# Kernel optimization log

Measured on AMD Instinct MI355X. Metric: run time of the kernel, lower is better.

## Reference

```python
import jax, jax.numpy as jnp
import numpy as np

N_NODES = 100000
N_EDGES = 1600000
N_GRAPHS = 1024
DIM_IN = 128
DIM_SELF = 16
BN_EPS = 1e-5


def _bn(x, gamma, beta):
    # training-mode BatchNorm1d over dim 0 (biased variance, as torch uses for normalization)
    m = jnp.mean(x, axis=0)
    v = jnp.mean((x - m) ** 2, axis=0)
    return gamma * (x - m) * jax.lax.rsqrt(v + BN_EPS) + beta


def _mlp(x, W1, b1, g, b, W2, b2):
    h = x @ W1 + b1
    h = jax.nn.relu(_bn(h, g, b))
    return h @ W2 + b2


def _gin(h, src, dst, W1, b1, g, b, W2, b2):
    # GINConv with eps=0: (1+eps)*h + sum over in-neighbors, then MLP
    agg = jax.ops.segment_sum(h[src], dst, num_segments=N_NODES)
    return _mlp(h + agg, W1, b1, g, b, W2, b2)


def setup_inputs() -> dict:
    key = jax.random.key(0)
    ks = jax.random.split(key, 16)

    def lin(k, fan_in, fan_out):
        bound = 1.0 / np.sqrt(fan_in)
        k1, k2 = jax.random.split(k)
        W = jax.random.uniform(k1, (fan_in, fan_out), jnp.float32, -bound, bound)
        b = jax.random.uniform(k2, (fan_out,), jnp.float32, -bound, bound)
        return W, b

    inp = {}
    inp['feat'] = jax.random.normal(ks[0], (N_NODES, DIM_IN), jnp.float32)
    inp['self_feat'] = jax.random.normal(ks[1], (N_GRAPHS, DIM_SELF), jnp.float32)
    inp['edge_src'] = jax.random.randint(ks[2], (N_EDGES,), 0, N_NODES, jnp.int32)
    inp['edge_dst'] = jax.random.randint(ks[3], (N_EDGES,), 0, N_NODES, jnp.int32)
    inp['node2graph'] = jnp.sort(jax.random.randint(ks[4], (N_NODES,), 0, N_GRAPHS, jnp.int32))

    inp['g1_W1'], inp['g1_b1'] = lin(ks[5], DIM_IN, 100)
    inp['g1_gamma'] = jnp.ones((100,), jnp.float32)
    inp['g1_beta'] = jnp.zeros((100,), jnp.float32)
    inp['g1_W2'], inp['g1_b2'] = lin(ks[6], 100, 100)

    inp['g2_W1'], inp['g2_b1'] = lin(ks[7], 100, 20)
    inp['g2_gamma'] = jnp.ones((20,), jnp.float32)
    inp['g2_beta'] = jnp.zeros((20,), jnp.float32)
    inp['g2_W2'], inp['g2_b2'] = lin(ks[8], 20, 20)

    inp['fc1_W'], inp['fc1_b'] = lin(ks[9], 20 * DIM_SELF, 32)
    inp['bn1_gamma'] = jnp.ones((32,), jnp.float32)
    inp['bn1_beta'] = jnp.zeros((32,), jnp.float32)
    inp['fc2_W'], inp['fc2_b'] = lin(ks[10], 32, 8)
    inp['bn2_gamma'] = jnp.ones((8,), jnp.float32)
    inp['bn2_beta'] = jnp.zeros((8,), jnp.float32)
    inp['fc3_W'], inp['fc3_b'] = lin(ks[11], 8, 1)
    return inp


def reference(feat, self_feat,
              g1_W1, g1_b1, g1_gamma, g1_beta, g1_W2, g1_b2,
              g2_W1, g2_b1, g2_gamma, g2_beta, g2_W2, g2_b2,
              fc1_W, fc1_b, bn1_gamma, bn1_beta,
              fc2_W, fc2_b, bn2_gamma, bn2_beta,
              fc3_W, fc3_b,
              edge_src, edge_dst, node2graph):
    h = _gin(feat, edge_src, edge_dst, g1_W1, g1_b1, g1_gamma, g1_beta, g1_W2, g1_b2)
    h = jax.nn.relu(h)
    h = _gin(h, edge_src, edge_dst, g2_W1, g2_b1, g2_gamma, g2_beta, g2_W2, g2_b2)
    h = jax.nn.relu(h)  # [N, 20]

    # dgl.mean_nodes: per-graph mean of node features
    sums = jax.ops.segment_sum(h, node2graph, num_segments=N_GRAPHS)  # [B, 20]
    cnts = jax.ops.segment_sum(jnp.ones((N_NODES,), h.dtype), node2graph, num_segments=N_GRAPHS)
    hg = sums / jnp.maximum(cnts, 1.0)[:, None]

    # kronecker fusion: bmm([B,20,1],[B,1,dim_self]) -> flatten
    kron = jnp.einsum('bi,bj->bij', hg, self_feat).reshape(N_GRAPHS, -1)  # [B, 20*dim_self]

    out = jax.nn.relu(_bn(kron @ fc1_W + fc1_b, bn1_gamma, bn1_beta))
    # dropout(0.3) is identity in eval mode
    out = jax.nn.relu(_bn(out @ fc2_W + fc2_b, bn2_gamma, bn2_beta))
    out = out @ fc3_W + fc3_b  # [B, dim_out]
    return out
```

## Files before the change

### kernel.cpp

```cpp
#include <hip/hip_runtime.h>

#define NN 100000
#define NE 1600000
#define NG 1024
#define DIN 128
#define D1 100
#define D2 20
#define DSELF 16
#define BN_EPS 1e-5f

#define NB 391
#define NBLK 782
#define EPB 2048
#define RAWCAP 5120
#define NAGG2 4000
#define NREP 64
#define APITCH 136

typedef unsigned int uint;
typedef unsigned short ushort;
typedef __attribute__((ext_vector_type(8))) short bfv8;
typedef __attribute__((ext_vector_type(4))) float fv4;

__device__ inline float bflo(uint x) { return __uint_as_float(x << 16); }
__device__ inline float bfhi(uint x) { return __uint_as_float(x & 0xffff0000u); }
__device__ inline float bfval(ushort h) { return __uint_as_float(((uint)h) << 16); }
__device__ inline uint packbf2(float a, float b) {
    uint ua = __float_as_uint(a), ub = __float_as_uint(b);
    ua += 0x7fffu + ((ua >> 16) & 1u);
    ub += 0x7fffu + ((ub >> 16) & 1u);
    return (ua >> 16) | (ub & 0xffff0000u);
}
__device__ inline ushort bfr(float x) {
    uint u = __float_as_uint(x);
    u += 0x7fffu + ((u >> 16) & 1u);
    return (ushort)(u >> 16);
}

__global__ __launch_bounds__(256) void k_gemm1(const float* __restrict__ feat,
                                               const float* __restrict__ W1,
                                               ushort* __restrict__ z1bf,
                                               float* __restrict__ pb1r) {
    __shared__ __align__(16) char smem[64 * APITCH * 2 + 112 * APITCH * 2];
    ushort* Al = (ushort*)smem;
    ushort* Bt = (ushort*)(smem + 64 * APITCH * 2);
    int t = threadIdx.x;
    if (blockIdx.x == 0) {
        for (int i = t; i < NREP * 200; i += 256) pb1r[i] = 0.f;
    }
    int row0 = blockIdx.x * 64;
#pragma unroll
    for (int i = 0; i < 8; i++) {
        int p = i * 256 + t;
        int r = p >> 5, cq = p & 31;
        int row = row0 + r; if (row >= NN) row = NN - 1;
        float4 v = *(const float4*)(feat + (size_t)row * DIN + cq * 4);
        ushort* dst = Al + r * APITCH + 4 * cq;
        dst[0] = bfr(v.x); dst[1] = bfr(v.y); dst[2] = bfr(v.z); dst[3] = bfr(v.w);
    }
    for (int p = t; p < 12800; p += 256) {
        int k = p / 100, n = p % 100;
        Bt[n * APITCH + k] = bfr(W1[p]);
    }
    __syncthreads();
    int w = __builtin_amdgcn_readfirstlane(t >> 6);
    int l = t & 63;
    int m16 = l & 15, quad = l >> 4;
    fv4 acc[7];
#pragma unroll
    for (int nt = 0; nt < 7; nt++) acc[nt] = (fv4){0.f, 0.f, 0.f, 0.f};
    const ushort* arow = Al + (w * 16 + m16) * APITCH;
#pragma unroll
    for (int kk = 0; kk < 4; kk++) {
        int kb = kk * 32 + quad * 8;
        bfv8 a = *(const bfv8*)(arow + kb);
#pragma unroll
        for (int nt = 0; nt < 7; nt++) {
            bfv8 b = *(const bfv8*)(Bt + (nt * 16 + m16) * APITCH + kb);
            acc[nt] = __builtin_amdgcn_mfma_f32_16x16x32_bf16(a, b, acc[nt], 0, 0, 0);
        }
    }
    __syncthreads();
    float* Ep = (float*)smem;
#pragma unroll
    for (int nt = 0; nt < 7; nt++) {
        int n = nt * 16 + m16;
        if (n < 100) {
#pragma unroll
            for (int rix = 0; rix < 4; rix++)
                Ep[(w * 16 + quad * 4 + rix) * 101 + n] = acc[nt][rix];
        }
    }
    __syncthreads();
#pragma unroll
    for (int i = 0; i < 13; i++) {
        int p = i * 256 + t;
        if (p < 3200) {
            int rr = p / 50, cc = 2 * (p % 50);
            int row = row0 + rr;
            if (row < NN) {
                float v0 = Ep[rr * 101 + cc], v1 = Ep[rr * 101 + cc + 1];
                *(uint*)(z1bf + (size_t)row * 128 + cc) = packbf2(v0, v1);
            }
        }
    }
}

__global__ __launch_bounds__(256) void k_csrA1(const int* __restrict__ dst,
                                               int* __restrict__ pbcount,
                                               const float* __restrict__ W2,
                                               const float* __restrict__ W1p,
                                               ushort* __restrict__ W2fh,
                                               ushort* __restrict__ W2fl,
                                               ushort* __restrict__ W1pfh,
                                               ushort* __restrict__ W1pfl) {
    __shared__ int h[NB];
    int t = threadIdx.x, blk = blockIdx.x;
    if (blk < 9) {
#pragma unroll
        for (int i2 = 0; i2 < 8; i2++) {
            int idx = blk * 2048 + i2 * 256 + t;
            int l = (idx >> 3) & 63, j = idx & 7;
            int kq = (l >> 4) * 8 + j;
            int n16 = l & 15;
            if (idx < 14336) {
                int tile = idx >> 9; int nt = tile >> 2, kk = tile & 3;
                int k = kk * 32 + kq, n = nt * 16 + n16;
                float v = (k < 100 && n < 100) ? W2[k * 100 + n] : 0.f;
                ushort hh = bfr(v);
                W2fh[idx] = hh; W2fl[idx] = bfr(v - bfval(hh));
            } else {
                int idx2 = idx - 14336;
                int tile = idx2 >> 9; int nt = tile >> 2, kk = tile & 3;
                int k = kk * 32 + kq, n = nt * 16 + n16;
                float v = (k < 100 && n < 20) ? W1p[k * 20 + n] : 0.f;
                ushort hh = bfr(v);
                W1pfh[idx2] = hh; W1pfl[idx2] = bfr(v - bfval(hh));
            }
        }
    }
    for (int i = t; i < NB; i += 256) h[i] = 0;
    __syncthreads();
    int e0 = blk * EPB + t;
#pragma unroll
    for (int i = 0; i < 8; i++) {
        int e = e0 + i * 256;
        if (e < NE) atomicAdd(&h[dst[e] >> 8], 1);
    }
    __syncthreads();
    for (int i = t; i < NB; i += 256) pbcount[i * NBLK + blk] = h[i];
}

__global__ __launch_bounds__(1024) void k_csrS1(int* __restrict__ pbcount,
                                                int* __restrict__ btot) {
    __shared__ int s[1024];
    int t = threadIdx.x, b = blockIdx.x;
    int v = (t < NBLK) ? pbcount[b * NBLK + t] : 0;
    s[t] = v;
    __syncthreads();
    for (int off = 1; off < 1024; off <<= 1) {
        int x = (t >= off) ? s[t - off] : 0;
        __syncthreads();
        s[t] += x;
        __syncthreads();
    }
    if (t < NBLK) pbcount[b * NBLK + t] = s[t] - v;
    if (t == 1023) btot[b] = s[t];
}

__global__ __launch_bounds__(256) void k_csrA2(const int* __restrict__ src,
                                               const int* __restrict__ dst,
                                               const int* __restrict__ pbexcl,
                                               const int* __restrict__ btot,
                                               int* __restrict__ ebase_g,
                                               uint* __restrict__ gbuf) {
    __shared__ int cur[NB];
    __shared__ int sa[512], sb[512];
    int t = threadIdx.x, blk = blockIdx.x;
    int o0 = (t < NB) ? btot[t] : 0;
    int o1 = (t + 256 < NB) ? btot[t + 256] : 0;
    sa[t] = o0; sa[t + 256] = o1;
    __syncthreads();
    int* sp = sa; int* dp = sb;
    for (int off = 1; off < 512; off <<= 1) {
        dp[t] = sp[t] + ((t >= off) ? sp[t - off] : 0);
        int i2 = t + 256;
        dp[i2] = sp[i2] + ((i2 >= off) ? sp[i2 - off] : 0);
        __syncthreads();
        int* tmp = sp; sp = dp; dp = tmp;
    }
    if (t < NB)       cur[t]       = (sp[t] - o0) + pbexcl[t * NBLK + blk];
    if (t + 256 < NB) cur[t + 256] = (sp[t + 256] - o1) + pbexcl[(t + 256) * NBLK + blk];
    if (blk == 0) {
        if (t < NB)       ebase_g[t]       = sp[t] - o0;
        if (t + 256 < NB) ebase_g[t + 256] = sp[t + 256] - o1;
        if (t == 0)       ebase_g[NB]      = sp[NB - 1];
    }
    __syncthreads();
    int e0 = blk * EPB + t;
#pragma unroll
    for (int i = 0; i < 8; i++) {
        int e = e0 + i * 256;
        if (e < NE) {
            int d = dst[e];
            int b = d >> 8;
            int pos = atomicAdd(&cur[b], 1);
            gbuf[pos] = (uint)src[e] | ((uint)(d & 255) << 17);
        }
    }
}

__global__ __launch_bounds__(256) void k_csrB(const uint* __restrict__ gbuf,
                                              const int* __restrict__ ebase,
                                              int* __restrict__ deg,
                                              int* __restrict__ offs,
                                              int* __restrict__ srcS) {
    __shared__ uint raw[RAWCAP];
    __shared__ int srt[RAWCAP];
    __shared__ int pref[256], cur[256];
    int t = threadIdx.x, b = blockIdx.x;
    int e0 = ebase[b], e1 = ebase[b + 1];
    int cnt = e1 - e0; if (cnt > RAWCAP) cnt = RAWCAP;
    cur[t] = 0;
    for (int i = t; i < cnt; i += 256) raw[i] = gbuf[e0 + i];
    __syncthreads();
    for (int i = t; i < cnt; i += 256) atomicAdd(&cur[raw[i] >> 17], 1);
    __syncthreads();
    int v = cur[t];
    pref[t] = v;
    __syncthreads();
    for (int off = 1; off < 256; off <<= 1) {
        int x = (t >= off) ? pref[t - off] : 0;
        __syncthreads();
        pref[t] += x;
        __syncthreads();
    }
    int excl = pref[t] - v;
    int node = b * 256 + t;
    if (node < NN) { deg[node] = v; offs[node] = e0 + excl; }
    cur[t] = excl;
    __syncthreads();
    for (int i = t; i < cnt; i += 256) {
        uint p = raw[i];
        int lpos = atomicAdd(&cur[p >> 17], 1);
        srt[lpos] = (int)(p & 0x1FFFFu);
    }
    __syncthreads();
    for (int i = t; i < cnt; i += 256) srcS[e0 + i] = srt[i];
}

__global__ __launch_bounds__(256) void k_agg1(const ushort* __restrict__ z1bf,
                                              const int* __restrict__ offs,
                                              const int* __restrict__ deg,
                                              const int* __restrict__ srcS,
                                              ushort* __restrict__ u1b,
                                              float* __restrict__ pb1r) {
    __shared__ float part[4][200];
    int t = threadIdx.x;
    int wv = __builtin_amdgcn_readfirstlane(t >> 6);
    int l = t & 63;
    bool act = l < 50;
    const ushort* zc = z1bf + 2 * l;
    float S0 = 0.f, S1 = 0.f, Q0 = 0.f, Q1 = 0.f;
    int n0 = blockIdx.x * 16 + wv * 4;
#pragma unroll 1
    for (int k = 0; k < 4; k++) {
        int n = n0 + k;
        int d = deg[n], base = offs[n];
        float a0 = 0.f, a1 = 0.f, b0 = 0.f, b1 = 0.f;
        float c0 = 0.f, c1 = 0.f, e0 = 0.f, e1 = 0.f;
        int i = 0;
        for (; i + 8 <= d; i += 8) {
            int s0 = srcS[base + i],     s1 = srcS[base + i + 1];
            int s2 = srcS[base + i + 2], s3 = srcS[base + i + 3];
            int s4 = srcS[base + i + 4], s5 = srcS[base + i + 5];
            int s6 = srcS[base + i + 6], s7 = srcS[base + i + 7];
            if (act) {
                uint x0 = *(const uint*)(zc + (size_t)s0 * 128);
                uint x1 = *(const uint*)(zc + (size_t)s1 * 128);
                uint x2 = *(const uint*)(zc + (size_t)s2 * 128);
                uint x3 = *(const uint*)(zc + (size_t)s3 * 128);
                uint x4 = *(const uint*)(zc + (size_t)s4 * 128);
                uint x5 = *(const uint*)(zc + (size_t)s5 * 128);
                uint x6 = *(const uint*)(zc + (size_t)s6 * 128);
                uint x7 = *(const uint*)(zc + (size_t)s7 * 128);
                a0 += bflo(x0); a1 += bfhi(x0);
                b0 += bflo(x1); b1 += bfhi(x1);
                c0 += bflo(x2); c1 += bfhi(x2);
                e0 += bflo(x3); e1 += bfhi(x3);
                a0 += bflo(x4); a1 += bfhi(x4);
                b0 += bflo(x5); b1 += bfhi(x5);
                c0 += bflo(x6); c1 += bfhi(x6);
                e0 += bflo(x7); e1 += bfhi(x7);
            }
        }
        for (; i + 2 <= d; i += 2) {
            int s0 = srcS[base + i], s1 = srcS[base + i + 1];
            if (act) {
                uint x0 = *(const uint*)(zc + (size_t)s0 * 128);
                uint x1 = *(const uint*)(zc + (size_t)s1 * 128);
                a0 += bflo(x0); a1 += bfhi(x0);
                b0 += bflo(x1); b1 += bfhi(x1);
            }
        }
        if (i < d) {
            int s0 = srcS[base + i];
            if (act) {
                uint x0 = *(const uint*)(zc + (size_t)s0 * 128);
                a0 += bflo(x0); a1 += bfhi(x0);
            }
        }
        if (act) {
            uint xs = *(const uint*)(zc + (size_t)n * 128);
            float r0 = (a0 + b0) + (c0 + e0) + bflo(xs);
            float r1 = (a1 + b1) + (c1 + e1) + bfhi(xs);
            *(uint*)(u1b + (size_t)n * 100 + 2 * l) = packbf2(r0, r1);
            S0 += r0; S1 += r1;
            Q0 = fmaf(r0, r0, Q0); Q1 = fmaf(r1, r1, Q1);
        }
    }
    if (act) {
        part[wv][2 * l] = S0;        part[wv][2 * l + 1] = S1;
        part[wv][100 + 2 * l] = Q0;  part[wv][100 + 2 * l + 1] = Q1;
    }
    __syncthreads();
    if (t < 200) {
        float s = part[0][t] + part[1][t] + part[2][t] + part[3][t];
        atomicAdd(&pb1r[(blockIdx.x & (NREP - 1)) * 200 + t], s);
    }
}

__global__ __launch_bounds__(256) void k_m2(const ushort* __restrict__ u1b,
                                            const float* __restrict__ pb1r,
                                            const float* __restrict__ gamma,
                                            const float* __restrict__ beta,
                                            const ushort* __restrict__ W2fh,
                                            const ushort* __restrict__ W2fl,
                                            const float* __restrict__ b2,
                                            const ushort* __restrict__ W1pfh,
                                            const ushort* __restrict__ W1pfl,
                                            ushort* __restrict__ z2bf,
                                            float* __restrict__ pb2r,
                                            float* __restrict__ hgsum) {
    __shared__ __align__(16) ushort Ah[64 * APITCH];
    __shared__ __align__(16) ushort Alo[64 * APITCH];
    __shared__ float red200[200];
    __shared__ float scW[100], shW[100];
    int t = threadIdx.x;
    if (blockIdx.x == 0) {
        for (int i = t; i < NREP * 40; i += 256) pb2r[i] = 0.f;
        for (int i = t; i < NG * D2; i += 256) hgsum[i] = 0.f;
    }
    if (t < 200) {
        float s = 0.f;
#pragma unroll 8
        for (int r = 0; r < NREP; r++) s += pb1r[r * 200 + t];
        red200[t] = s;
    }
    for (int p = t; p < 896; p += 256) {
        int r = p / 14, c = 100 + 2 * (p % 14);
        *(uint*)(Ah + r * APITCH + c) = 0u;
        *(uint*)(Alo + r * APITCH + c) = 0u;
    }
    __syncthreads();
    if (t < 100) {
        float S = red200[t], Q = red200[100 + t];
        float mean = S * (1.f / NN);
        float var = Q * (1.f / NN) - mean * mean;
        float inv = rsqrtf(var + BN_EPS);
        float s = gamma[t] * inv;
        scW[t] = s;
        shW[t] = beta[t] - mean * s;
    }
    __syncthreads();
    int row0 = blockIdx.x * 64;
#pragma unroll
    for (int i = 0; i < 13; i++) {
        int p = i * 256 + t;
        if (p < 3200) {
            int r = p / 50, c = 2 * (p % 50);
            int row = row0 + r; if (row >= NN) row = NN - 1;
            uint x = *(const uint*)(u1b + (size_t)row * 100 + c);
            float y0 = fmaxf(bflo(x) * scW[c] + shW[c], 0.f);
            float y1 = fmaxf(bfhi(x) * scW[c + 1] + shW[c + 1], 0.f);
            ushort h0 = bfr(y0), h1 = bfr(y1);
            ushort l0 = bfr(y0 - bfval(h0)), l1 = bfr(y1 - bfval(h1));
            *(uint*)(Ah + r * APITCH + c) = (uint)h0 | ((uint)h1 << 16);
            *(uint*)(Alo + r * APITCH + c) = (uint)l0 | ((uint)l1 << 16);
        }
    }
    __syncthreads();
    int w = __builtin_amdgcn_readfirstlane(t >> 6);
    int l = t & 63;
    int m16 = l & 15, quad = l >> 4;
    fv4 acc[7];
#pragma unroll
    for (int nt = 0; nt < 7; nt++) acc[nt] = (fv4){0.f, 0.f, 0.f, 0.f};
    {
        const ushort* arH = Ah + (w * 16 + m16) * APITCH;
        const ushort* arL = Alo + (w * 16 + m16) * APITCH;
#pragma unroll
        for (int kk = 0; kk < 4; kk++) {
            int kb = kk * 32 + quad * 8;
            bfv8 ah = *(const bfv8*)(arH + kb);
            bfv8 al = *(const bfv8*)(arL + kb);
#pragma unroll
            for (int nt = 0; nt < 7; nt++) {
                int fo = ((nt * 4 + kk) << 9) + l * 8;
                bfv8 bh = *(const bfv8*)(W2fh + fo);
                bfv8 bl = *(const bfv8*)(W2fl + fo);
                acc[nt] = __builtin_amdgcn_mfma_f32_16x16x32_bf16(ah, bh, acc[nt], 0, 0, 0);
                acc[nt] = __builtin_amdgcn_mfma_f32_16x16x32_bf16(ah, bl, acc[nt], 0, 0, 0);
                acc[nt] = __builtin_amdgcn_mfma_f32_16x16x32_bf16(al, bh, acc[nt], 0, 0, 0);
            }
        }
    }
    __syncthreads();
#pragma unroll
    for (int nt = 0; nt < 7; nt++) {
        int n = nt * 16 + m16;
        float bb = (n < 100) ? b2[n] : 0.f;
#pragma unroll
        for (int rix = 0; rix < 4; rix++) {
            int r = w * 16 + quad * 4 + rix;
            float hv = (n < 100) ? fmaxf(acc[nt][rix] + bb, 0.f) : 0.f;
            ushort hh = bfr(hv);
            Ah[r * APITCH + n] = hh;
            Alo[r * APITCH + n] = bfr(hv - bfval(hh));
        }
    }
    __syncthreads();
    fv4 acc2[2];
    acc2[0] = (fv4){0.f, 0.f, 0.f, 0.f};
    acc2[1] = (fv4){0.f, 0.f, 0.f, 0.f};
    {
        const ushort* arH = Ah + (w * 16 + m16) * APITCH;
        const ushort* arL = Alo + (w * 16 + m16) * APITCH;
#pragma unroll
        for (int kk = 0; kk < 4; kk++) {
            int kb = kk * 32 + quad * 8;
            bfv8 ah = *(const bfv8*)(arH + kb);
            bfv8 al = *(const bfv8*)(arL + kb);
#pragma unroll
            for (int nt = 0; nt < 2; nt++) {
                int fo = ((nt * 4 + kk) << 9) + l * 8;
                bfv8 bh = *(const bfv8*)(W1pfh + fo);
                bfv8 bl = *(const bfv8*)(W1pfl + fo);
                acc2[nt] = __builtin_amdgcn_mfma_f32_16x16x32_bf16(ah, bh, acc2[nt], 0, 0, 0);
                acc2[nt] = __builtin_amdgcn_mfma_f32_16x16x32_bf16(ah, bl, acc2[nt], 0, 0, 0);
                acc2[nt] = __builtin_amdgcn_mfma_f32_16x16x32_bf16(al, bh, acc2[nt], 0, 0, 0);
            }
        }
    }
#pragma unroll
    for (int nt = 0; nt < 2; nt++) {
        int c = nt * 16 + m16;
        if (c < 20) {
#pragma unroll
            for (int rix = 0; rix < 4; rix++) {
                int row = row0 + w * 16 + quad * 4 + rix;
                if (row < NN) z2bf[(size_t)row * 32 + c] = bfr(acc2[nt][rix]);
            }
        }
    }
}

__global__ __launch_bounds__(256) void k_agg2(const ushort* __restrict__ z2bf,
                                              const int* __restrict__ offs,
                                              const int* __restrict__ deg,
                                              const int* __restrict__ srcS,
                                              float* __restrict__ u2,
                                              float* __restrict__ pb2r) {
    __shared__ float ls[500], lq[500];
    int t = threadIdx.x;
    int n = blockIdx.x * 25 + t / 10;
    int c2 = 2 * (t % 10);
    float r0 = 0.f, r1 = 0.f;
    if (t < 250 && n < NN) {
        int d = deg[n], base = offs[n];
        const ushort* zc = z2bf + c2;
        float a0 = 0.f, a1 = 0.f, b0 = 0.f, b1 = 0.f;
        int i = 0;
        for (; i + 2 <= d; i += 2) {
            uint x0 = *(const uint*)(zc + (size_t)srcS[base + i] * 32);
            uint x1 = *(const uint*)(zc + (size_t)srcS[base + i + 1] * 32);
            a0 += bflo(x0); a1 += bfhi(x0);
            b0 += bflo(x1); b1 += bfhi(x1);
        }
        if (i < d) {
            uint x0 = *(const uint*)(zc + (size_t)srcS[base + i] * 32);
            a0 += bflo(x0); a1 += bfhi(x0);
        }
        uint xs = *(const uint*)(zc + (size_t)n * 32);
        r0 = a0 + b0 + bflo(xs);
        r1 = a1 + b1 + bfhi(xs);
        *(float2*)(u2 + (size_t)n * D2 + c2) = make_float2(r0, r1);
    }
    if (t < 250) {
        int idx = (t / 10) * 20 + c2;
        ls[idx] = r0;     lq[idx] = r0 * r0;
        ls[idx + 1] = r1; lq[idx + 1] = r1 * r1;
    }
    __syncthreads();
    if (t < 20) {
        float S = 0.f, Q = 0.f;
#pragma unroll
        for (int j = 0; j < 25; j++) { S += ls[j * 20 + t]; Q += lq[j * 20 + t]; }
        int rep = (blockIdx.x & (NREP - 1)) * 40;
        atomicAdd(&pb2r[rep + t], S);
        atomicAdd(&pb2r[rep + 20 + t], Q);
    }
}

__global__ __launch_bounds__(256) void k_m3p(const float* __restrict__ u2,
                                             const float* __restrict__ pb2r,
                                             const float* __restrict__ gamma,
                                             const float* __restrict__ beta,
                                             const float* __restrict__ W2p,
                                             const float* __restrict__ b2p,
                                             const int* __restrict__ n2g,
                                             float* __restrict__ hgsum) {
    __shared__ float X[256][21];
    __shared__ int gl[256];
    __shared__ float red40[40], scB[20], shB[20];
    int t = threadIdx.x;
    if (t < 40) {
        float s = 0.f;
#pragma unroll 8
        for (int r = 0; r < NREP; r++) s += pb2r[r * 40 + t];
        red40[t] = s;
    }
    __syncthreads();
    if (t < 20) {
        float S = red40[t], Q = red40[20 + t];
        float mean = S * (1.f / NN);
        float var = Q * (1.f / NN) - mean * mean;
        float inv = rsqrtf(var + BN_EPS);
        float s = gamma[t] * inv;
        scB[t] = s;
        shB[t] = beta[t] - mean * s;
    }
    __syncthreads();
    int row = blockIdx.x * 256 + t;
    bool valid = row < NN;
    gl[t] = valid ? n2g[row] : -1;
    if (valid) {
        float ya[20];
        const float4* up = (const float4*)(u2 + (size_t)row * D2);
#pragma unroll
        for (int i = 0; i < 5; i++) {
            float4 v = up[i];
            ya[4 * i + 0] = fmaxf(v.x * scB[4 * i + 0] + shB[4 * i + 0], 0.f);
            ya[4 * i + 1] = fmaxf(v.y * scB[4 * i + 1] + shB[4 * i + 1], 0.f);
            ya[4 * i + 2] = fmaxf(v.z * scB[4 * i + 2] + shB[4 * i + 2], 0.f);
            ya[4 * i + 3] = fmaxf(v.w * scB[4 * i + 3] + shB[4 * i + 3], 0.f);
        }
#pragma unroll
        for (int j = 0; j < D2; j++) {
            float h = b2p[j];
#pragma unroll
            for (int k = 0; k < D2; k++) h = fmaf(ya[k], W2p[k * D2 + j], h);
            X[t][j] = fmaxf(h, 0.f);
        }
    } else {
#pragma unroll
        for (int j = 0; j < D2; j++) X[t][j] = 0.f;
    }
    __syncthreads();
    if (t < 160) {
        int seg = t / 20, j = t % 20;
        int i0 = seg * 32, i1 = i0 + 32;
        int gprev = -2;
        float acc = 0.f;
        for (int i = i0; i < i1; i++) {
            int gi = gl[i];
            if (gi != gprev) {
                if (gprev >= 0) atomicAdd(&hgsum[gprev * D2 + j], acc);
                gprev = gi; acc = 0.f;
            }
            acc += X[i][j];
        }
        if (gprev >= 0) atomicAdd(&hgsum[gprev * D2 + j], acc);
    }
}

__global__ void k_head1(const float* __restrict__ hgsum, const int* __restrict__ n2g,
                        const float* __restrict__ sf,
                        const float* __restrict__ fc1W, float* __restrict__ a1) {
    int b = blockIdx.x * 8 + threadIdx.x / 32;
    int c = threadIdx.x % 32;
    if (b >= NG) return;
    int lo = 0, hi2 = NN;
    while (lo < hi2) { int mid = (lo + hi2) >> 1; if (n2g[mid] < b) lo = mid + 1; else hi2 = mid; }
    int s0 = lo;
    hi2 = NN;
    while (lo < hi2) { int mid = (lo + hi2) >> 1; if (n2g[mid] < b + 1) lo = mid + 1; else hi2 = mid; }
    float rc = 1.f / fmaxf((float)(lo - s0), 1.f);
    const float* hgb = hgsum + b * D2;
    const float* sfb = sf + b * DSELF;
    float acc = 0.f;
    for (int i = 0; i < D2; i++) {
        float hv = hgb[i] * rc;
#pragma unroll
        for (int j = 0; j < DSELF; j++)
            acc += hv * sfb[j] * fc1W[(i * DSELF + j) * 32 + c];
    }
    a1[b * 32 + c] = acc;
}

__global__ __launch_bounds__(1024) void k_head2(
    const float* __restrict__ a1, const float* __restrict__ g1,
    const float* __restrict__ be1, const float* __restrict__ fc2W,
    const float* __restrict__ g2, const float* __restrict__ be2,
    const float* __restrict__ fc3W, const float* __restrict__ fc3b,
    float* __restrict__ out) {
    int t = threadIdx.x;
    int lane = t & 63, w = t >> 6;
    __shared__ float s1[16][32], s2[16][32];
    __shared__ float sc[32], sh[32], sc2[8], sh2[8];
    float x[32];
    const float4* ap = (const float4*)(a1 + t * 32);
#pragma unroll
    for (int i = 0; i < 8; i++) {
        float4 v = ap[i];
        x[4 * i] = v.x; x[4 * i + 1] = v.y; x[4 * i + 2] = v.z; x[4 * i + 3] = v.w;
    }
#pragma unroll
    for (int c = 0; c < 32; c++) {
        float v = x[c], q = v * v;
        for (int o = 32; o > 0; o >>= 1) {
            v += __shfl_down(v, o, 64);
            q += __shfl_down(q, o, 64);
        }
        if (lane == 0) { s1[w][c] = v; s2[w][c] = q; }
    }
    __syncthreads();
    if (t < 32) {
        float s = 0.f, q = 0.f;
        for (int ww = 0; ww < 16; ww++) { s += s1[ww][t]; q += s2[ww][t]; }
        float mean = s * (1.f / NG);
        float var = q * (1.f / NG) - mean * mean;
        float inv = rsqrtf(var + BN_EPS);
        float scl = g1[t] * inv;
        sc[t] = scl;
        sh[t] = be1[t] - mean * scl;
    }
    __syncthreads();
#pragma unroll
    for (int c = 0; c < 32; c++) x[c] = fmaxf(x[c] * sc[c] + sh[c], 0.f);
    float y[8];
#pragma unroll
    for (int p = 0; p < 8; p++) {
        float a = 0.f;
#pragma unroll
        for (int c = 0; c < 32; c++) a += x[c] * fc2W[c * 8 + p];
        y[p] = a;
    }
    __syncthreads();
#pragma unroll
    for (int p = 0; p < 8; p++) {
        float v = y[p], q = v * v;
        for (int o = 32; o > 0; o >>= 1) {
            v += __shfl_down(v, o, 64);
            q += __shfl_down(q, o, 64);
        }
        if (lane == 0) { s1[w][p] = v; s2[w][p] = q; }
    }
    __syncthreads();
    if (t < 8) {
        float s = 0.f, q = 0.f;
        for (int ww = 0; ww < 16; ww++) { s += s1[ww][t]; q += s2[ww][t]; }
        float mean = s * (1.f / NG);
        float var = q * (1.f / NG) - mean * mean;
        float inv = rsqrtf(var + BN_EPS);
        float scl = g2[t] * inv;
        sc2[t] = scl;
        sh2[t] = be2[t] - mean * scl;
    }
    __syncthreads();
    float o = fc3b[0];
#pragma unroll
    for (int p = 0; p < 8; p++) {
        float yy = fmaxf(y[p] * sc2[p] + sh2[p], 0.f);
        o += yy * fc3W[p];
    }
    out[t] = o;
}

extern "C" void kernel_launch(void* const* d_in, const int* in_sizes, int n_in,
                              void* d_out, int out_size, void* d_ws, size_t ws_size,
                              hipStream_t stream) {
    const float* feat    = (const float*)d_in[0];
    const float* sf      = (const float*)d_in[1];
    const int*   esrc    = (const int*)d_in[2];
    const int*   edst    = (const int*)d_in[3];
    const int*   n2g     = (const int*)d_in[4];
    const float* g1W1    = (const float*)d_in[5];
    const float* g1gam   = (const float*)d_in[7];
    const float* g1bet   = (const float*)d_in[8];
    const float* g1W2    = (const float*)d_in[9];
    const float* g1b2    = (const float*)d_in[10];
    const float* g2W1    = (const float*)d_in[11];
    const float* g2gam   = (const float*)d_in[13];
    const float* g2bet   = (const float*)d_in[14];
    const float* g2W2    = (const float*)d_in[15];
    const float* g2b2    = (const float*)d_in[16];
    const float* fc1W    = (const float*)d_in[17];
    const float* hbn1g   = (const float*)d_in[19];
    const float* hbn1b   = (const float*)d_in[20];
    const float* fc2W    = (const float*)d_in[21];
    const float* hbn2g   = (const float*)d_in[23];
    const float* hbn2b   = (const float*)d_in[24];
    const float* fc3W    = (const float*)d_in[25];
    const float* fc3b    = (const float*)d_in[26];
    float* out = (float*)d_out;

    char* w = (char*)d_ws;
    size_t off = 0;
    auto alloc = [&](size_t bytes) -> char* {
        char* p = w + off;
        off += (bytes + 15) & ~(size_t)15;
        return p;
    };
    char* regA = alloc((size_t)NN * 128 * 2);
    ushort* z1bf = (ushort*)regA;
    ushort* z2bf = (ushort*)regA;
    float*  u2   = (float*)(regA + 6400000);
    ushort* u1b  = (ushort*)alloc((size_t)NN * 100 * 2);
    int*   pbcnt = (int*)alloc((size_t)NB * NBLK * 4);
    int*   btot  = (int*)alloc(NB * 4);
    int*   ebase = (int*)alloc((NB + 1) * 4);
    uint*  gbuf  = (uint*)alloc((size_t)NE * 4);
    int*   deg   = (int*)alloc(NN * 4);
    int*   offs  = (int*)alloc(NN * 4);
    int*   srcS  = (int*)alloc((size_t)NE * 4);
    float* pb1r  = (float*)alloc((size_t)NREP * 200 * 4);
    float* pb2r  = (float*)alloc((size_t)NREP * 40 * 4);
    ushort* W2fh = (ushort*)alloc(14336 * 2);
    ushort* W2fl = (ushort*)alloc(14336 * 2);
    ushort* W1pfh = (ushort*)alloc(4096 * 2);
    ushort* W1pfl = (ushort*)alloc(4096 * 2);
    float* hgsum = (float*)alloc((size_t)NG * D2 * 4);
    float* a1    = (float*)alloc(NG * 32 * 4);
    (void)in_sizes; (void)n_in; (void)out_size; (void)ws_size;

    k_gemm1<<<(NN + 63) / 64, 256, 0, stream>>>(feat, g1W1, z1bf, pb1r);

    k_csrA1<<<NBLK, 256, 0, stream>>>(edst, pbcnt, g1W2, g2W1, W2fh, W2fl, W1pfh, W1pfl);
    k_csrS1<<<NB, 1024, 0, stream>>>(pbcnt, btot);
    k_csrA2<<<NBLK, 256, 0, stream>>>(esrc, edst, pbcnt, btot, ebase, gbuf);
    k_csrB<<<NB, 256, 0, stream>>>(gbuf, ebase, deg, offs, srcS);

    k_agg1<<<NN / 16, 256, 0, stream>>>(z1bf, offs, deg, srcS, u1b, pb1r);

    k_m2<<<(NN + 63) / 64, 256, 0, stream>>>(u1b, pb1r, g1gam, g1bet, W2fh, W2fl, g1b2,
                                             W1pfh, W1pfl, z2bf, pb2r, hgsum);

    k_agg2<<<NAGG2, 256, 0, stream>>>(z2bf, offs, deg, srcS, u2, pb2r);
    k_m3p<<<(NN + 255) / 256, 256, 0, stream>>>(u2, pb2r, g2gam, g2bet, g2W2, g2b2, n2g, hgsum);

    k_head1<<<NG / 8, 256, 0, stream>>>(hgsum, n2g, sf, fc1W, a1);
    k_head2<<<1, 1024, 0, stream>>>(a1, hbn1g, hbn1b, fc2W, hbn2g, hbn2b, fc3W, fc3b, out);
}
```

Baseline: 394.7 us.

## Split layer-1 features into column halves, fuse gemm1 with CSR histogram

The bf16 layer-1 table is stored as two 50-column halves with a 64-element row pitch, and the gather-sum runs as two passes. Each pass uses all 64 lanes by splitting a node's edges across two half-waves and combining them with a cross-lane shuffle. The goal is a smaller, more cache-resident gather working set per pass and better lane utilisation. The CSR histogram and weight-prep blocks are merged into the gemm1 launch to save a launch and let the two overlap, and agg2 gets an 8-way unrolled edge loop for more memory-level parallelism. The cost is reading the edge lists twice and an extra kernel launch for the second aggregation pass.

```diff
diff --git a/kernel.cpp b/kernel.cpp
--- a/kernel.cpp
+++ b/kernel.cpp
@@ -16,6 +16,7 @@
 #define NAGG2 4000
 #define NREP 64
 #define APITCH 136
+#define G1BLK 1563
 
 typedef unsigned int uint;
 typedef unsigned short ushort;
@@ -37,18 +38,66 @@
     return (ushort)(u >> 16);
 }
 
-__global__ __launch_bounds__(256) void k_gemm1(const float* __restrict__ feat,
-                                               const float* __restrict__ W1,
-                                               ushort* __restrict__ z1bf,
-                                               float* __restrict__ pb1r) {
+__global__ __launch_bounds__(256) void k_gemm1A1(const float* __restrict__ feat,
+                                                 const float* __restrict__ W1,
+                                                 ushort* __restrict__ z1a,
+                                                 ushort* __restrict__ z1b,
+                                                 float* __restrict__ pb1r,
+                                                 const int* __restrict__ edst,
+                                                 int* __restrict__ pbcount,
+                                                 const float* __restrict__ W2,
+                                                 const float* __restrict__ W1p,
+                                                 ushort* __restrict__ W2fh,
+                                                 ushort* __restrict__ W2fl,
+                                                 ushort* __restrict__ W1pfh,
+                                                 ushort* __restrict__ W1pfl) {
     __shared__ __align__(16) char smem[64 * APITCH * 2 + 112 * APITCH * 2];
+    int t = threadIdx.x;
+    int blk = blockIdx.x;
+    if (blk >= G1BLK) {
+        int hb = blk - G1BLK;
+        int* h = (int*)smem;
+        if (hb < 9) {
+#pragma unroll
+            for (int i2 = 0; i2 < 8; i2++) {
+                int idx = hb * 2048 + i2 * 256 + t;
+                int l = (idx >> 3) & 63, j = idx & 7;
+                int kq = (l >> 4) * 8 + j;
+                int n16 = l & 15;
+                if (idx < 14336) {
+                    int tile = idx >> 9; int nt = tile >> 2, kk = tile & 3;
+                    int k = kk * 32 + kq, n = nt * 16 + n16;
+                    float v = (k < 100 && n < 100) ? W2[k * 100 + n] : 0.f;
+                    ushort hh = bfr(v);
+                    W2fh[idx] = hh; W2fl[idx] = bfr(v - bfval(hh));
+                } else {
+                    int idx2 = idx - 14336;
+                    int tile = idx2 >> 9; int nt = tile >> 2, kk = tile & 3;
+                    int k = kk * 32 + kq, n = nt * 16 + n16;
+                    float v = (k < 100 && n < 20) ? W1p[k * 20 + n] : 0.f;
+                    ushort hh = bfr(v);
+                    W1pfh[idx2] = hh; W1pfl[idx2] = bfr(v - bfval(hh));
+                }
+            }
+        }
+        for (int i = t; i < NB; i += 256) h[i] = 0;
+        __syncthreads();
+        int e0 = hb * EPB + t;
+#pragma unroll
+        for (int i = 0; i < 8; i++) {
+            int e = e0 + i * 256;
+            if (e < NE) atomicAdd(&h[edst[e] >> 8], 1);
+        }
+        __syncthreads();
+        for (int i = t; i < NB; i += 256) pbcount[i * NBLK + hb] = h[i];
+        return;
+    }
     ushort* Al = (ushort*)smem;
     ushort* Bt = (ushort*)(smem + 64 * APITCH * 2);
-    int t = threadIdx.x;
-    if (blockIdx.x == 0) {
+    if (blk == 0) {
         for (int i = t; i < NREP * 200; i += 256) pb1r[i] = 0.f;
     }
-    int row0 = blockIdx.x * 64;
+    int row0 = blk * 64;
 #pragma unroll
     for (int i = 0; i < 8; i++) {
         int p = i * 256 + t;
@@ -99,56 +148,12 @@
             int rr = p / 50, cc = 2 * (p % 50);
             int row = row0 + rr;
             if (row < NN) {
-                float v0 = Ep[rr * 101 + cc], v1 = Ep[rr * 101 + cc + 1];
-                *(uint*)(z1bf + (size_t)row * 128 + cc) = packbf2(v0, v1);
-            }
-        }
-    }
-}
-
-__global__ __launch_bounds__(256) void k_csrA1(const int* __restrict__ dst,
-                                               int* __restrict__ pbcount,
-                                               const float* __restrict__ W2,
-                                               const float* __restrict__ W1p,
-                                               ushort* __restrict__ W2fh,
-                                               ushort* __restrict__ W2fl,
-                                               ushort* __restrict__ W1pfh,
-                                               ushort* __restrict__ W1pfl) {
-    __shared__ int h[NB];
-    int t = threadIdx.x, blk = blockIdx.x;
-    if (blk < 9) {
-#pragma unroll
-        for (int i2 = 0; i2 < 8; i2++) {
-            int idx = blk * 2048 + i2 * 256 + t;
-            int l = (idx >> 3) & 63, j = idx & 7;
-            int kq = (l >> 4) * 8 + j;
-            int n16 = l & 15;
-            if (idx < 14336) {
-                int tile = idx >> 9; int nt = tile >> 2, kk = tile & 3;
-                int k = kk * 32 + kq, n = nt * 16 + n16;
-                float v = (k < 100 && n < 100) ? W2[k * 100 + n] : 0.f;
-                ushort hh = bfr(v);
-                W2fh[idx] = hh; W2fl[idx] = bfr(v - bfval(hh));
-            } else {
-                int idx2 = idx - 14336;
-                int tile = idx2 >> 9; int nt = tile >> 2, kk = tile & 3;
-                int k = kk * 32 + kq, n = nt * 16 + n16;
-                float v = (k < 100 && n < 20) ? W1p[k * 20 + n] : 0.f;
-                ushort hh = bfr(v);
-                W1pfh[idx2] = hh; W1pfl[idx2] = bfr(v - bfval(hh));
-            }
-        }
-    }
-    for (int i = t; i < NB; i += 256) h[i] = 0;
-    __syncthreads();
-    int e0 = blk * EPB + t;
-#pragma unroll
-    for (int i = 0; i < 8; i++) {
-        int e = e0 + i * 256;
-        if (e < NE) atomicAdd(&h[dst[e] >> 8], 1);
-    }
-    __syncthreads();
-    for (int i = t; i < NB; i += 256) pbcount[i * NBLK + blk] = h[i];
+                uint pk = packbf2(Ep[rr * 101 + cc], Ep[rr * 101 + cc + 1]);
+                if (cc < 50) *(uint*)(z1a + (size_t)row * 64 + cc) = pk;
+                else         *(uint*)(z1b + (size_t)row * 64 + (cc - 50)) = pk;
+            }
+        }
+    }
 }
 
 __global__ __launch_bounds__(1024) void k_csrS1(int* __restrict__ pbcount,
@@ -249,18 +254,21 @@
     for (int i = t; i < cnt; i += 256) srcS[e0 + i] = srt[i];
 }
 
-__global__ __launch_bounds__(256) void k_agg1(const ushort* __restrict__ z1bf,
+__global__ __launch_bounds__(256) void k_agg1(const ushort* __restrict__ tab,
                                               const int* __restrict__ offs,
                                               const int* __restrict__ deg,
                                               const int* __restrict__ srcS,
                                               ushort* __restrict__ u1b,
-                                              float* __restrict__ pb1r) {
-    __shared__ float part[4][200];
+                                              float* __restrict__ pb1r,
+                                              int cbase) {
+    __shared__ float part[4][100];
     int t = threadIdx.x;
     int wv = __builtin_amdgcn_readfirstlane(t >> 6);
     int l = t & 63;
-    bool act = l < 50;
-    const ushort* zc = z1bf + 2 * l;
+    int p = l >> 5;
+    int c = l & 31;
+    bool act = c < 25;
+    const ushort* zc = tab + 2 * c;
     float S0 = 0.f, S1 = 0.f, Q0 = 0.f, Q1 = 0.f;
     int n0 = blockIdx.x * 16 + wv * 4;
 #pragma unroll 1
@@ -271,62 +279,59 @@
         float c0 = 0.f, c1 = 0.f, e0 = 0.f, e1 = 0.f;
         int i = 0;
         for (; i + 8 <= d; i += 8) {
-            int s0 = srcS[base + i],     s1 = srcS[base + i + 1];
-            int s2 = srcS[base + i + 2], s3 = srcS[base + i + 3];
-            int s4 = srcS[base + i + 4], s5 = srcS[base + i + 5];
-            int s6 = srcS[base + i + 6], s7 = srcS[base + i + 7];
+            int sa = srcS[base + i + p];
+            int sb = srcS[base + i + 2 + p];
+            int sc = srcS[base + i + 4 + p];
+            int sd = srcS[base + i + 6 + p];
             if (act) {
-                uint x0 = *(const uint*)(zc + (size_t)s0 * 128);
-                uint x1 = *(const uint*)(zc + (size_t)s1 * 128);
-                uint x2 = *(const uint*)(zc + (size_t)s2 * 128);
-                uint x3 = *(const uint*)(zc + (size_t)s3 * 128);
-                uint x4 = *(const uint*)(zc + (size_t)s4 * 128);
-                uint x5 = *(const uint*)(zc + (size_t)s5 * 128);
-                uint x6 = *(const uint*)(zc + (size_t)s6 * 128);
-                uint x7 = *(const uint*)(zc + (size_t)s7 * 128);
+                uint x0 = *(const uint*)(zc + (size_t)sa * 64);
+                uint x1 = *(const uint*)(zc + (size_t)sb * 64);
+                uint x2 = *(const uint*)(zc + (size_t)sc * 64);
+                uint x3 = *(const uint*)(zc + (size_t)sd * 64);
                 a0 += bflo(x0); a1 += bfhi(x0);
                 b0 += bflo(x1); b1 += bfhi(x1);
                 c0 += bflo(x2); c1 += bfhi(x2);
                 e0 += bflo(x3); e1 += bfhi(x3);
-                a0 += bflo(x4); a1 += bfhi(x4);
-                b0 += bflo(x5); b1 += bfhi(x5);
-                c0 += bflo(x6); c1 += bfhi(x6);
-                e0 += bflo(x7); e1 += bfhi(x7);
             }
         }
         for (; i + 2 <= d; i += 2) {
-            int s0 = srcS[base + i], s1 = srcS[base + i + 1];
+            int sa = srcS[base + i + p];
             if (act) {
-                uint x0 = *(const uint*)(zc + (size_t)s0 * 128);
-                uint x1 = *(const uint*)(zc + (size_t)s1 * 128);
+                uint x0 = *(const uint*)(zc + (size_t)sa * 64);
                 a0 += bflo(x0); a1 += bfhi(x0);
-                b0 += bflo(x1); b1 += bfhi(x1);
             }
         }
         if (i < d) {
-            int s0 = srcS[base + i];
-            if (act) {
-                uint x0 = *(const uint*)(zc + (size_t)s0 * 128);
-                a0 += bflo(x0); a1 += bfhi(x0);
-            }
-        }
-        if (act) {
-            uint xs = *(const uint*)(zc + (size_t)n * 128);
-            float r0 = (a0 + b0) + (c0 + e0) + bflo(xs);
-            float r1 = (a1 + b1) + (c1 + e1) + bfhi(xs);
-            *(uint*)(u1b + (size_t)n * 100 + 2 * l) = packbf2(r0, r1);
+            int sa = srcS[base + i];
+            if (act && p == 0) {
+                uint x0 = *(const uint*)(zc + (size_t)sa * 64);
+                b0 += bflo(x0); b1 += bfhi(x0);
+            }
+        }
+        if (act && p == 1) {
+            uint xs = *(const uint*)(zc + (size_t)n * 64);
+            b0 += bflo(xs); b1 += bfhi(xs);
+        }
+        float r0 = (a0 + b0) + (c0 + e0);
+        float r1 = (a1 + b1) + (c1 + e1);
+        r0 += __shfl_xor(r0, 32, 64);
+        r1 += __shfl_xor(r1, 32, 64);
+        if (act && p == 0) {
+            *(uint*)(u1b + (size_t)n * 100 + cbase + 2 * c) = packbf2(r0, r1);
             S0 += r0; S1 += r1;
             Q0 = fmaf(r0, r0, Q0); Q1 = fmaf(r1, r1, Q1);
         }
     }
-    if (act) {
-        part[wv][2 * l] = S0;        part[wv][2 * l + 1] = S1;
-        part[wv][100 + 2 * l] = Q0;  part[wv][100 + 2 * l + 1] = Q1;
-    }
-    __syncthreads();
-    if (t < 200) {
+    if (act && p == 0) {
+        part[wv][2 * c] = S0;       part[wv][2 * c + 1] = S1;
+        part[wv][50 + 2 * c] = Q0;  part[wv][51 + 2 * c] = Q1;
+    }
+    __syncthreads();
+    if (t < 100) {
         float s = part[0][t] + part[1][t] + part[2][t] + part[3][t];
-        atomicAdd(&pb1r[(blockIdx.x & (NREP - 1)) * 200 + t], s);
+        int rep = (blockIdx.x & (NREP - 1)) * 200;
+        int dst = (t < 50) ? (rep + cbase + t) : (rep + 100 + cbase + (t - 50));
+        atomicAdd(&pb1r[dst], s);
     }
 }
 
@@ -480,7 +485,30 @@
         int d = deg[n], base = offs[n];
         const ushort* zc = z2bf + c2;
         float a0 = 0.f, a1 = 0.f, b0 = 0.f, b1 = 0.f;
+        float c0 = 0.f, c1 = 0.f, e0 = 0.f, e1 = 0.f;
         int i = 0;
+        for (; i + 8 <= d; i += 8) {
+            int s0 = srcS[base + i],     s1 = srcS[base + i + 1];
+            int s2 = srcS[base + i + 2], s3 = srcS[base + i + 3];
+            int s4 = srcS[base + i + 4], s5 = srcS[base + i + 5];
+            int s6 = srcS[base + i + 6], s7 = srcS[base + i + 7];
+            uint x0 = *(const uint*)(zc + (size_t)s0 * 32);
+            uint x1 = *(const uint*)(zc + (size_t)s1 * 32);
+            uint x2 = *(const uint*)(zc + (size_t)s2 * 32);
+            uint x3 = *(const uint*)(zc + (size_t)s3 * 32);
+            uint x4 = *(const uint*)(zc + (size_t)s4 * 32);
+            uint x5 = *(const uint*)(zc + (size_t)s5 * 32);
+            uint x6 = *(const uint*)(zc + (size_t)s6 * 32);
+            uint x7 = *(const uint*)(zc + (size_t)s7 * 32);
+            a0 += bflo(x0); a1 += bfhi(x0);
+            b0 += bflo(x1); b1 += bfhi(x1);
+            c0 += bflo(x2); c1 += bfhi(x2);
+            e0 += bflo(x3); e1 += bfhi(x3);
+            a0 += bflo(x4); a1 += bfhi(x4);
+            b0 += bflo(x5); b1 += bfhi(x5);
+            c0 += bflo(x6); c1 += bfhi(x6);
+            e0 += bflo(x7); e1 += bfhi(x7);
+        }
         for (; i + 2 <= d; i += 2) {
             uint x0 = *(const uint*)(zc + (size_t)srcS[base + i] * 32);
             uint x1 = *(const uint*)(zc + (size_t)srcS[base + i + 1] * 32);
@@ -492,8 +520,8 @@
             a0 += bflo(x0); a1 += bfhi(x0);
         }
         uint xs = *(const uint*)(zc + (size_t)n * 32);
-        r0 = a0 + b0 + bflo(xs);
-        r1 = a1 + b1 + bfhi(xs);
+        r0 = (a0 + b0) + (c0 + e0) + bflo(xs);
+        r1 = (a1 + b1) + (c1 + e1) + bfhi(xs);
         *(float2*)(u2 + (size_t)n * D2 + c2) = make_float2(r0, r1);
     }
     if (t < 250) {
@@ -723,7 +751,8 @@
         return p;
     };
     char* regA = alloc((size_t)NN * 128 * 2);
-    ushort* z1bf = (ushort*)regA;
+    ushort* z1a = (ushort*)regA;
+    ushort* z1b = (ushort*)(regA + 12800000);
     ushort* z2bf = (ushort*)regA;
     float*  u2   = (float*)(regA + 6400000);
     ushort* u1b  = (ushort*)alloc((size_t)NN * 100 * 2);
@@ -744,17 +773,17 @@
     float* a1    = (float*)alloc(NG * 32 * 4);
     (void)in_sizes; (void)n_in; (void)out_size; (void)ws_size;
 
-    k_gemm1<<<(NN + 63) / 64, 256, 0, stream>>>(feat, g1W1, z1bf, pb1r);
-
-    k_csrA1<<<NBLK, 256, 0, stream>>>(edst, pbcnt, g1W2, g2W1, W2fh, W2fl, W1pfh, W1pfl);
+    k_gemm1A1<<<G1BLK + NBLK, 256, 0, stream>>>(feat, g1W1, z1a, z1b, pb1r, edst, pbcnt,
+                                                g1W2, g2W1, W2fh, W2fl, W1pfh, W1pfl);
     k_csrS1<<<NB, 1024, 0, stream>>>(pbcnt, btot);
     k_csrA2<<<NBLK, 256, 0, stream>>>(esrc, edst, pbcnt, btot, ebase, gbuf);
     k_csrB<<<NB, 256, 0, stream>>>(gbuf, ebase, deg, offs, srcS);
 
-    k_agg1<<<NN / 16, 256, 0, stream>>>(z1bf, offs, deg, srcS, u1b, pb1r);
-
-    k_m2<<<(NN + 63) / 64, 256, 0, stream>>>(u1b, pb1r, g1gam, g1bet, W2fh, W2fl, g1b2,
-                                             W1pfh, W1pfl, z2bf, pb2r, hgsum);
+    k_agg1<<<NN / 16, 256, 0, stream>>>(z1a, offs, deg, srcS, u1b, pb1r, 0);
+    k_agg1<<<NN / 16, 256, 0, stream>>>(z1b, offs, deg, srcS, u1b, pb1r, 50);
+
+    k_m2<<<G1BLK, 256, 0, stream>>>(u1b, pb1r, g1gam, g1bet, W2fh, W2fl, g1b2,
+                                    W1pfh, W1pfl, z2bf, pb2r, hgsum);
 
     k_agg2<<<NAGG2, 256, 0, stream>>>(z2bf, offs, deg, srcS, u2, pb2r);
     k_m3p<<<(NN + 255) / 256, 256, 0, stream>>>(u2, pb2r, g2gam, g2bet, g2W2, g2b2, n2g, hgsum);
```

Measured after the change: 440.9 us. 1.12x slower.

## Merge gemm1 with CSR histogram, stage bucket scatter in LDS, unroll agg2 gathers

Applied to the files above, without the earlier changes.

Folds the dense first GEMM and the CSR histogram/weight-split kernel into one launch, with the extra blocks doing histogram work, so the two can overlap and one launch is removed. The CSR scatter kernel now sorts each block's edges by bucket in shared memory before writing, so global writes to gbuf land in contiguous runs instead of scattered atomically-placed positions. The second aggregation loop is unrolled by 8 with four accumulators to keep more gathers in flight. This costs extra LDS and an additional local prefix scan per block.

```diff
diff --git a/kernel.cpp b/kernel.cpp
--- a/kernel.cpp
+++ b/kernel.cpp
@@ -16,6 +16,7 @@
 #define NAGG2 4000
 #define NREP 64
 #define APITCH 136
+#define G1BLK 1563
 
 typedef unsigned int uint;
 typedef unsigned short ushort;
@@ -37,18 +38,65 @@
     return (ushort)(u >> 16);
 }
 
-__global__ __launch_bounds__(256) void k_gemm1(const float* __restrict__ feat,
-                                               const float* __restrict__ W1,
-                                               ushort* __restrict__ z1bf,
-                                               float* __restrict__ pb1r) {
+__global__ __launch_bounds__(256) void k_gemm1A1(const float* __restrict__ feat,
+                                                 const float* __restrict__ W1,
+                                                 ushort* __restrict__ z1bf,
+                                                 float* __restrict__ pb1r,
+                                                 const int* __restrict__ edst,
+                                                 int* __restrict__ pbcount,
+                                                 const float* __restrict__ W2,
+                                                 const float* __restrict__ W1p,
+                                                 ushort* __restrict__ W2fh,
+                                                 ushort* __restrict__ W2fl,
+                                                 ushort* __restrict__ W1pfh,
+                                                 ushort* __restrict__ W1pfl) {
     __shared__ __align__(16) char smem[64 * APITCH * 2 + 112 * APITCH * 2];
+    int t = threadIdx.x;
+    int blk = blockIdx.x;
+    if (blk >= G1BLK) {
+        int hb = blk - G1BLK;
+        int* h = (int*)smem;
+        if (hb < 9) {
+#pragma unroll
+            for (int i2 = 0; i2 < 8; i2++) {
+                int idx = hb * 2048 + i2 * 256 + t;
+                int l = (idx >> 3) & 63, j = idx & 7;
+                int kq = (l >> 4) * 8 + j;
+                int n16 = l & 15;
+                if (idx < 14336) {
+                    int tile = idx >> 9; int nt = tile >> 2, kk = tile & 3;
+                    int k = kk * 32 + kq, n = nt * 16 + n16;
+                    float v = (k < 100 && n < 100) ? W2[k * 100 + n] : 0.f;
+                    ushort hh = bfr(v);
+                    W2fh[idx] = hh; W2fl[idx] = bfr(v - bfval(hh));
+                } else {
+                    int idx2 = idx - 14336;
+                    int tile = idx2 >> 9; int nt = tile >> 2, kk = tile & 3;
+                    int k = kk * 32 + kq, n = nt * 16 + n16;
+                    float v = (k < 100 && n < 20) ? W1p[k * 20 + n] : 0.f;
+                    ushort hh = bfr(v);
+                    W1pfh[idx2] = hh; W1pfl[idx2] = bfr(v - bfval(hh));
+                }
+            }
+        }
+        for (int i = t; i < NB; i += 256) h[i] = 0;
+        __syncthreads();
+        int e0 = hb * EPB + t;
+#pragma unroll
+        for (int i = 0; i < 8; i++) {
+            int e = e0 + i * 256;
+            if (e < NE) atomicAdd(&h[edst[e] >> 8], 1);
+        }
+        __syncthreads();
+        for (int i = t; i < NB; i += 256) pbcount[i * NBLK + hb] = h[i];
+        return;
+    }
     ushort* Al = (ushort*)smem;
     ushort* Bt = (ushort*)(smem + 64 * APITCH * 2);
-    int t = threadIdx.x;
-    if (blockIdx.x == 0) {
+    if (blk == 0) {
         for (int i = t; i < NREP * 200; i += 256) pb1r[i] = 0.f;
     }
-    int row0 = blockIdx.x * 64;
+    int row0 = blk * 64;
 #pragma unroll
     for (int i = 0; i < 8; i++) {
         int p = i * 256 + t;
@@ -106,51 +154,6 @@
     }
 }
 
-__global__ __launch_bounds__(256) void k_csrA1(const int* __restrict__ dst,
-                                               int* __restrict__ pbcount,
-                                               const float* __restrict__ W2,
-                                               const float* __restrict__ W1p,
-                                               ushort* __restrict__ W2fh,
-                                               ushort* __restrict__ W2fl,
-                                               ushort* __restrict__ W1pfh,
-                                               ushort* __restrict__ W1pfl) {
-    __shared__ int h[NB];
-    int t = threadIdx.x, blk = blockIdx.x;
-    if (blk < 9) {
-#pragma unroll
-        for (int i2 = 0; i2 < 8; i2++) {
-            int idx = blk * 2048 + i2 * 256 + t;
-            int l = (idx >> 3) & 63, j = idx & 7;
-            int kq = (l >> 4) * 8 + j;
-            int n16 = l & 15;
-            if (idx < 14336) {
-                int tile = idx >> 9; int nt = tile >> 2, kk = tile & 3;
-                int k = kk * 32 + kq, n = nt * 16 + n16;
-                float v = (k < 100 && n < 100) ? W2[k * 100 + n] : 0.f;
-                ushort hh = bfr(v);
-                W2fh[idx] = hh; W2fl[idx] = bfr(v - bfval(hh));
-            } else {
-                int idx2 = idx - 14336;
-                int tile = idx2 >> 9; int nt = tile >> 2, kk = tile & 3;
-                int k = kk * 32 + kq, n = nt * 16 + n16;
-                float v = (k < 100 && n < 20) ? W1p[k * 20 + n] : 0.f;
-                ushort hh = bfr(v);
-                W1pfh[idx2] = hh; W1pfl[idx2] = bfr(v - bfval(hh));
-            }
-        }
-    }
-    for (int i = t; i < NB; i += 256) h[i] = 0;
-    __syncthreads();
-    int e0 = blk * EPB + t;
-#pragma unroll
-    for (int i = 0; i < 8; i++) {
-        int e = e0 + i * 256;
-        if (e < NE) atomicAdd(&h[dst[e] >> 8], 1);
-    }
-    __syncthreads();
-    for (int i = t; i < NB; i += 256) pbcount[i * NBLK + blk] = h[i];
-}
-
 __global__ __launch_bounds__(1024) void k_csrS1(int* __restrict__ pbcount,
                                                 int* __restrict__ btot) {
     __shared__ int s[1024];
@@ -174,12 +177,18 @@
                                                const int* __restrict__ btot,
                                                int* __restrict__ ebase_g,
                                                uint* __restrict__ gbuf) {
-    __shared__ int cur[NB];
+    __shared__ int gb[NB];
+    __shared__ int lo[NB];
+    __shared__ int cnt[NB];
     __shared__ int sa[512], sb[512];
+    __shared__ uint stage[EPB];
+    __shared__ ushort bkts[EPB];
     int t = threadIdx.x, blk = blockIdx.x;
     int o0 = (t < NB) ? btot[t] : 0;
     int o1 = (t + 256 < NB) ? btot[t + 256] : 0;
     sa[t] = o0; sa[t + 256] = o1;
+    if (t < NB) cnt[t] = 0;
+    if (t + 256 < NB) cnt[t + 256] = 0;
     __syncthreads();
     int* sp = sa; int* dp = sb;
     for (int off = 1; off < 512; off <<= 1) {
@@ -189,8 +198,8 @@
         __syncthreads();
         int* tmp = sp; sp = dp; dp = tmp;
     }
-    if (t < NB)       cur[t]       = (sp[t] - o0) + pbexcl[t * NBLK + blk];
-    if (t + 256 < NB) cur[t + 256] = (sp[t + 256] - o1) + pbexcl[(t + 256) * NBLK + blk];
+    if (t < NB)       gb[t]       = (sp[t] - o0) + pbexcl[t * NBLK + blk];
+    if (t + 256 < NB) gb[t + 256] = (sp[t + 256] - o1) + pbexcl[(t + 256) * NBLK + blk];
     if (blk == 0) {
         if (t < NB)       ebase_g[t]       = sp[t] - o0;
         if (t + 256 < NB) ebase_g[t + 256] = sp[t + 256] - o1;
@@ -198,15 +207,48 @@
     }
     __syncthreads();
     int e0 = blk * EPB + t;
+    uint pv[8]; int bk[8];
 #pragma unroll
     for (int i = 0; i < 8; i++) {
         int e = e0 + i * 256;
         if (e < NE) {
             int d = dst[e];
-            int b = d >> 8;
-            int pos = atomicAdd(&cur[b], 1);
-            gbuf[pos] = (uint)src[e] | ((uint)(d & 255) << 17);
-        }
+            bk[i] = d >> 8;
+            pv[i] = (uint)src[e] | ((uint)(d & 255) << 17);
+            atomicAdd(&cnt[bk[i]], 1);
+        } else bk[i] = -1;
+    }
+    __syncthreads();
+    sa[t] = (t < NB) ? cnt[t] : 0;
+    sa[t + 256] = (t + 256 < NB) ? cnt[t + 256] : 0;
+    __syncthreads();
+    sp = sa; dp = sb;
+    for (int off = 1; off < 512; off <<= 1) {
+        dp[t] = sp[t] + ((t >= off) ? sp[t - off] : 0);
+        int i2 = t + 256;
+        dp[i2] = sp[i2] + ((i2 >= off) ? sp[i2 - off] : 0);
+        __syncthreads();
+        int* tmp = sp; sp = dp; dp = tmp;
+    }
+    if (t < NB)       lo[t]       = sp[t] - cnt[t];
+    if (t + 256 < NB) lo[t + 256] = sp[t + 256] - cnt[t + 256];
+    __syncthreads();
+    if (t < NB) cnt[t] = 0;
+    if (t + 256 < NB) cnt[t + 256] = 0;
+    __syncthreads();
+#pragma unroll
+    for (int i = 0; i < 8; i++) {
+        if (bk[i] >= 0) {
+            int lpos = lo[bk[i]] + atomicAdd(&cnt[bk[i]], 1);
+            stage[lpos] = pv[i];
+            bkts[lpos] = (ushort)bk[i];
+        }
+    }
+    __syncthreads();
+    int cntb = (blk * EPB + EPB <= NE) ? EPB : (NE - blk * EPB);
+    for (int i = t; i < cntb; i += 256) {
+        int b = bkts[i];
+        gbuf[gb[b] + (i - lo[b])] = stage[i];
     }
 }
 
@@ -480,7 +522,30 @@
         int d = deg[n], base = offs[n];
         const ushort* zc = z2bf + c2;
         float a0 = 0.f, a1 = 0.f, b0 = 0.f, b1 = 0.f;
+        float c0 = 0.f, c1 = 0.f, e0 = 0.f, e1 = 0.f;
         int i = 0;
+        for (; i + 8 <= d; i += 8) {
+            int s0 = srcS[base + i],     s1 = srcS[base + i + 1];
+            int s2 = srcS[base + i + 2], s3 = srcS[base + i + 3];
+            int s4 = srcS[base + i + 4], s5 = srcS[base + i + 5];
+            int s6 = srcS[base + i + 6], s7 = srcS[base + i + 7];
+            uint x0 = *(const uint*)(zc + (size_t)s0 * 32);
+            uint x1 = *(const uint*)(zc + (size_t)s1 * 32);
+            uint x2 = *(const uint*)(zc + (size_t)s2 * 32);
+            uint x3 = *(const uint*)(zc + (size_t)s3 * 32);
+            uint x4 = *(const uint*)(zc + (size_t)s4 * 32);
+            uint x5 = *(const uint*)(zc + (size_t)s5 * 32);
+            uint x6 = *(const uint*)(zc + (size_t)s6 * 32);
+            uint x7 = *(const uint*)(zc + (size_t)s7 * 32);
+            a0 += bflo(x0); a1 += bfhi(x0);
+            b0 += bflo(x1); b1 += bfhi(x1);
+            c0 += bflo(x2); c1 += bfhi(x2);
+            e0 += bflo(x3); e1 += bfhi(x3);
+            a0 += bflo(x4); a1 += bfhi(x4);
+            b0 += bflo(x5); b1 += bfhi(x5);
+            c0 += bflo(x6); c1 += bfhi(x6);
+            e0 += bflo(x7); e1 += bfhi(x7);
+        }
         for (; i + 2 <= d; i += 2) {
             uint x0 = *(const uint*)(zc + (size_t)srcS[base + i] * 32);
             uint x1 = *(const uint*)(zc + (size_t)srcS[base + i + 1] * 32);
@@ -492,8 +557,8 @@
             a0 += bflo(x0); a1 += bfhi(x0);
         }
         uint xs = *(const uint*)(zc + (size_t)n * 32);
-        r0 = a0 + b0 + bflo(xs);
-        r1 = a1 + b1 + bfhi(xs);
+        r0 = (a0 + b0) + (c0 + e0) + bflo(xs);
+        r1 = (a1 + b1) + (c1 + e1) + bfhi(xs);
         *(float2*)(u2 + (size_t)n * D2 + c2) = make_float2(r0, r1);
     }
     if (t < 250) {
@@ -744,17 +809,16 @@
     float* a1    = (float*)alloc(NG * 32 * 4);
     (void)in_sizes; (void)n_in; (void)out_size; (void)ws_size;
 
-    k_gemm1<<<(NN + 63) / 64, 256, 0, stream>>>(feat, g1W1, z1bf, pb1r);
-
-    k_csrA1<<<NBLK, 256, 0, stream>>>(edst, pbcnt, g1W2, g2W1, W2fh, W2fl, W1pfh, W1pfl);
+    k_gemm1A1<<<G1BLK + NBLK, 256, 0, stream>>>(feat, g1W1, z1bf, pb1r, edst, pbcnt,
+                                                g1W2, g2W1, W2fh, W2fl, W1pfh, W1pfl);
     k_csrS1<<<NB, 1024, 0, stream>>>(pbcnt, btot);
     k_csrA2<<<NBLK, 256, 0, stream>>>(esrc, edst, pbcnt, btot, ebase, gbuf);
     k_csrB<<<NB, 256, 0, stream>>>(gbuf, ebase, deg, offs, srcS);
 
     k_agg1<<<NN / 16, 256, 0, stream>>>(z1bf, offs, deg, srcS, u1b, pb1r);
 
-    k_m2<<<(NN + 63) / 64, 256, 0, stream>>>(u1b, pb1r, g1gam, g1bet, W2fh, W2fl, g1b2,
-                                             W1pfh, W1pfl, z2bf, pb2r, hgsum);
+    k_m2<<<G1BLK, 256, 0, stream>>>(u1b, pb1r, g1gam, g1bet, W2fh, W2fl, g1b2,
+                                    W1pfh, W1pfl, z2bf, pb2r, hgsum);
 
     k_agg2<<<NAGG2, 256, 0, stream>>>(z2bf, offs, deg, srcS, u2, pb2r);
     k_m3p<<<(NN + 255) / 256, 256, 0, stream>>>(u2, pb2r, g2gam, g2bet, g2W2, g2b2, n2g, hgsum);
```

Measured after the change: 372.9 us. 1.06x faster.
